# Kernel optimization log

Measured on AMD Instinct MI355X. Metric: run time of the kernel, lower is better.

The kernel has to match this reference:

```python
import jax, jax.numpy as jnp
import numpy as np
from jax import lax

N_CLASSES = 10
GTG_ITER = 30
GTG_TOL = 1e-3
PLB = 0.5
EPS = 1e-8
B = 4096
INTERM = 128
CHANNELS = [64, 128, 256, 512]
SIZES = [8, 8, 4, 4]
EMB_DIM = 512


def setup_inputs() -> dict:
    key = jax.random.key(0)
    ks = jax.random.split(key, 16)
    inp = {}
    for i, (c, s) in enumerate(zip(CHANNELS, SIZES)):
        inp[f"feat{i}"] = jax.random.normal(ks[i], (B, c, s, s), dtype=jnp.float32)
    inp["embedds"] = jax.random.normal(ks[4], (B, EMB_DIM), dtype=jnp.float32)
    inp["outs"] = jax.random.normal(ks[5], (B, N_CLASSES), dtype=jnp.float32)
    inp["labels"] = jax.random.randint(ks[6], (B,), 0, N_CLASSES)
    for i, c in enumerate(CHANNELS):
        inp[f"ls_w{i}"] = jax.random.normal(ks[7 + i], (c, INTERM), dtype=jnp.float32) / np.sqrt(c).astype(np.float32)
        inp[f"ls_b{i}"] = jnp.zeros((INTERM,), dtype=jnp.float32)
    in_feat = GTG_ITER * N_CLASSES  # 300
    inp["mlp_w1"] = jax.random.normal(ks[11], (in_feat, in_feat // 2), dtype=jnp.float32) / np.sqrt(in_feat).astype(np.float32)
    inp["mlp_b1"] = jnp.zeros((in_feat // 2,), dtype=jnp.float32)
    inp["mlp_w2"] = jax.random.normal(ks[12], (in_feat // 2, in_feat // 4), dtype=jnp.float32) / np.sqrt(in_feat // 2).astype(np.float32)
    inp["mlp_b2"] = jnp.zeros((in_feat // 4,), dtype=jnp.float32)
    inp["mlp_w3"] = jax.random.normal(ks[13], (in_feat // 4 * 4, 1), dtype=jnp.float32) / np.sqrt(in_feat).astype(np.float32)
    inp["mlp_b3"] = jnp.zeros((1,), dtype=jnp.float32)
    return inp


def _make_A(emb):
    # get_A_cos_sim: normalize -> NN^T -> zero diag -> clamp[0,1]
    n = emb / jnp.maximum(jnp.linalg.norm(emb, axis=-1, keepdims=True), 1e-12)
    A = n @ n.T
    A = A * (1.0 - jnp.eye(A.shape[0], dtype=A.dtype))
    A = jnp.clip(A, 0.0, 1.0)
    # threshold strategy 'mean': zero entries below mean(A)
    A = jnp.where(A < jnp.mean(A), 0.0, A)
    # AM_strategy 'diversity': A = 1 - A
    return 1.0 - A


def _gtg(A, X0):
    # graph transduction game; while-loop emulated via scan with a running flag
    def step(carry, _):
        X, running = carry
        mult = X * (A @ X)                                 # [B,C]
        div = mult / (jnp.sum(mult, axis=1, keepdims=True) + EPS)
        X_new = X + div
        div_d = lax.stop_gradient(div)
        ent = -jnp.sum(div_d * jnp.log(div_d + EPS), axis=1)  # entropy, detached
        err = jnp.linalg.norm(div_d - lax.stop_gradient(X))
        X_out = jnp.where(running, X_new, X)
        xs_t = jnp.where(running, X_new, jnp.zeros_like(X_new))
        ent_t = jnp.where(running, ent, jnp.zeros_like(ent))
        return (X_out, jnp.logical_and(running, err > GTG_TOL)), (xs_t, ent_t)

    (_, _), (Xs, ents) = lax.scan(step, (X0, jnp.array(True)), None, length=GTG_ITER)
    return jnp.transpose(Xs, (1, 2, 0)), ents.T  # [B,C,T], [B,T]


def _ls(feat, w, b):
    # AvgPool2d over full spatial + Linear + ReLU
    pooled = jnp.mean(feat, axis=(2, 3))  # [B, n_c]
    return jax.nn.relu(pooled @ w + b)


def _mlp(xs_list, w1, b1, w2, b2, w3, b3):
    outs = []
    for xs in xs_list:
        x = xs.reshape(xs.shape[0], -1)  # [B, C*T], torch .view order
        x = jax.nn.relu(x @ w1 + b1)
        x = jax.nn.relu(x @ w2 + b2)
        outs.append(x)
    return (jnp.concatenate(outs, axis=1) @ w3 + b3)[:, 0]


def _init_X(labels, batch):
    n_lab = int(batch * PLB)
    X0 = jnp.full((batch, N_CLASSES), 1.0 / N_CLASSES, dtype=jnp.float32)
    X0 = X0.at[:n_lab].set(0.0)
    X0 = X0.at[jnp.arange(n_lab), labels[:n_lab]].set(1.0)
    return X0, n_lab


def reference(feat0, feat1, feat2, feat3, embedds, outs, labels,
              ls_w0, ls_b0, ls_w1, ls_b1, ls_w2, ls_b2, ls_w3, ls_b3,
              mlp_w1, mlp_b1, mlp_w2, mlp_b2, mlp_w3, mlp_b3):
    batch = embedds.shape[0]
    X0, n_lab = _init_X(labels, batch)
    feats = [feat0, feat1, feat2, feat3]
    lws = [ls_w0, ls_w1, ls_w2, ls_w3]
    lbs = [ls_b0, ls_b1, ls_b2, ls_b3]
    xs_list = []
    for f, w, b in zip(feats, lws, lbs):
        emb = _ls(f, w, b)
        Xs, _ = _gtg(_make_A(emb), X0)
        xs_list.append(Xs)
    y_pred = _mlp(xs_list, mlp_w1, mlp_b1, mlp_w2, mlp_b2, mlp_w3, mlp_b3)  # [B]
    _, ents = _gtg(_make_A(embedds), X0)
    y_true = jnp.mean(ents, axis=1)  # ent_strategy 'mean'
    labelled_mask = jnp.arange(batch) < n_lab
    return y_pred, y_true, labelled_mask
```

## Files before the change

### kernel.cpp

```cpp
#include <hip/hip_runtime.h>
#include <hip/hip_fp16.h>

typedef _Float16 f16x8 __attribute__((ext_vector_type(8)));
typedef float f32x4 __attribute__((ext_vector_type(4)));
typedef unsigned char uchar;

static __device__ __forceinline__ long long mk64(unsigned lo, unsigned hi)
{
    return (long long)(((unsigned long long)hi << 32) | (unsigned long long)lo);
}

static __device__ __forceinline__ int xfrag_off(int c, int j)
{
    return (j >> 6) * 1024 + (((j >> 3) & 3) * 16 + c) * 16 + ((j >> 5) & 1) * 8 + (j & 7);
}

static __device__ __forceinline__ int xsfrag_off(int row, int k)
{
    return (row >> 4) * 5120 + (k >> 5) * 512 + (((k >> 3) & 3) * 16 + (row & 15)) * 8 + (k & 7);
}

#define T03 0x24201800u
#define T47 0x2E2C2A28u
#define T8B 0x33323130u
#define TCF 0x37363534u

static __device__ __forceinline__ void expand4(unsigned w, unsigned& o0, unsigned& o1)
{
    unsigned even = w & 0x0F0F0F0Fu;
    unsigned odd  = (w >> 4) & 0x0F0F0F0Fu;
    unsigned i_lo = __builtin_amdgcn_perm(odd, even, 0x05010400u);
    unsigned i_hi = __builtin_amdgcn_perm(odd, even, 0x07030602u);
    {
        unsigned i3 = i_lo & 0x07070707u;
        unsigned ta = __builtin_amdgcn_perm(T47, T03, i3);
        unsigned tb = __builtin_amdgcn_perm(TCF, T8B, i3);
        unsigned m  = ((i_lo >> 3) & 0x01010101u) * 0xFFu;
        o0 = ta ^ ((ta ^ tb) & m);
    }
    {
        unsigned i3 = i_hi & 0x07070707u;
        unsigned ta = __builtin_amdgcn_perm(T47, T03, i3);
        unsigned tb = __builtin_amdgcn_perm(TCF, T8B, i3);
        unsigned m  = ((i_hi >> 3) & 0x01010101u) * 0xFFu;
        o1 = ta ^ ((ta ^ tb) & m);
    }
}

__global__ __launch_bounds__(256) void fused_ls_kernel(
    const float* __restrict__ f0, const float* __restrict__ f1,
    const float* __restrict__ f2, const float* __restrict__ f3,
    const float* __restrict__ embedds,
    const float* __restrict__ lw0, const float* __restrict__ lb0,
    const float* __restrict__ lw1, const float* __restrict__ lb1,
    const float* __restrict__ lw2, const float* __restrict__ lb2,
    const float* __restrict__ lw3, const float* __restrict__ lb3,
    __half* __restrict__ N16all, int pbase)
{
    __shared__ float pl[512];
    __shared__ float red[4];
    const int t = threadIdx.x;
    const int p = pbase + (blockIdx.x >> 12);
    const int row = blockIdx.x & 4095;

    if (p == 4) {
        float2 v = *(const float2*)(embedds + (size_t)row * 512 + t * 2);
        float ss = v.x * v.x + v.y * v.y;
        for (int off = 32; off > 0; off >>= 1) ss += __shfl_down(ss, off, 64);
        if ((t & 63) == 0) red[t >> 6] = ss;
        __syncthreads();
        float inv = 1.0f / fmaxf(sqrtf(red[0] + red[1] + red[2] + red[3]), 1e-12f);
        __half2 o;
        o.x = __float2half(v.x * inv);
        o.y = __float2half(v.y * inv);
        *(__half2*)(N16all + 2097152 + (size_t)row * 512 + t * 2) = o;
        return;
    }

    const float* feat; const float* w; const float* b; int C;
    switch (p) {
        case 0:  feat = f0; w = lw0; b = lb0; C = 64;  break;
        case 1:  feat = f1; w = lw1; b = lb1; C = 128; break;
        case 2:  feat = f2; w = lw2; b = lb2; C = 256; break;
        default: feat = f3; w = lw3; b = lb3; C = 512; break;
    }
    const float* fr = feat + (size_t)row * C * ((p < 2) ? 64 : 16);

    if (p == 0) {
        const int c = t >> 2, q = t & 3;
        const float4* src = (const float4*)(fr + c * 64 + q * 16);
        float s = 0.f;
#pragma unroll
        for (int i = 0; i < 4; ++i) { float4 v = src[i]; s += v.x + v.y + v.z + v.w; }
        s += __shfl_xor(s, 1, 64);
        s += __shfl_xor(s, 2, 64);
        if (q == 0) pl[c] = s * (1.0f / 64.f);
    } else if (p == 1) {
        const int c = t >> 1, h = t & 1;
        const float4* src = (const float4*)(fr + c * 64 + h * 32);
        float s = 0.f;
#pragma unroll
        for (int i = 0; i < 8; ++i) { float4 v = src[i]; s += v.x + v.y + v.z + v.w; }
        s += __shfl_xor(s, 1, 64);
        if (h == 0) pl[c] = s * (1.0f / 64.f);
    } else if (p == 2) {
        const float4* src = (const float4*)(fr + t * 16);
        float s = 0.f;
#pragma unroll
        for (int i = 0; i < 4; ++i) { float4 v = src[i]; s += v.x + v.y + v.z + v.w; }
        pl[t] = s * (1.0f / 16.f);
    } else {
#pragma unroll
        for (int cc = 0; cc < 2; ++cc) {
            const int c = t + cc * 256;
            const float4* src = (const float4*)(fr + c * 16);
            float s = 0.f;
#pragma unroll
            for (int i = 0; i < 4; ++i) { float4 v = src[i]; s += v.x + v.y + v.z + v.w; }
            pl[c] = s * (1.0f / 16.f);
        }
    }
    __syncthreads();

    float v = 0.f, ss = 0.f;
    if (t < 128) {
        float acc = b[t];
        for (int k = 0; k < C; ++k) acc = fmaf(pl[k], w[(size_t)k * 128 + t], acc);
        v = fmaxf(acc, 0.f);
        ss = v * v;
        for (int off = 32; off > 0; off >>= 1) ss += __shfl_down(ss, off, 64);
        if ((t & 63) == 0) red[t >> 6] = ss;
    }
    __syncthreads();
    if (t < 128) {
        float inv = 1.0f / fmaxf(sqrtf(red[0] + red[1]), 1e-12f);
        N16all[(size_t)p * 524288 + (size_t)row * 128 + t] = __float2half(v * inv);
    }
}

__global__ __launch_bounds__(256) void a_gemm_all(const __half* __restrict__ N16all,
                                                  __half* __restrict__ A16f,
                                                  float* __restrict__ partials,
                                                  int pbase)
{
    __shared__ __half smem[16384];
    __shared__ float reds[4];
    __half* As = smem;
    __half* Bs = smem + 8192;
    char* Cb = (char*)smem;
    const int t = threadIdx.x;
    const int lane = t & 63, wave = t >> 6;
    const int lp = blockIdx.x >> 10;
    const int p = pbase + lp;
    const int blk = blockIdx.x & 1023;
    const int K = (p == 4) ? 512 : 128;
    const __half* N16 = N16all + ((p == 4) ? 2097152u : (unsigned)p * 524288u);
    const int bx = blk & 31, by = blk >> 5;
    const int wr = wave >> 1, wc = wave & 1;
    const int fr = lane & 15;
    const int g = lane >> 4;
    const int r0 = by * 128, c0 = bx * 128;
    const int sr = t >> 3;
    const int sc = t & 7;

    f32x4 acc[4][4];
#pragma unroll
    for (int i = 0; i < 4; ++i)
#pragma unroll
        for (int j = 0; j < 4; ++j) acc[i][j] = (f32x4){0.f, 0.f, 0.f, 0.f};

    for (int kt = 0; kt < (K >> 6); ++kt) {
        const int kb = kt * 64;
        __syncthreads();
#pragma unroll
        for (int pp = 0; pp < 4; ++pp) {
            const int r = pp * 32 + sr;
            uint4 va = *(const uint4*)(N16 + (size_t)(r0 + r) * K + kb + sc * 8);
            uint4 vb = *(const uint4*)(N16 + (size_t)(c0 + r) * K + kb + sc * 8);
            const int d = r * 64 + ((((sc * 16) ^ ((r & 7) << 4))) >> 1);
            *(uint4*)&As[d] = va;
            *(uint4*)&Bs[d] = vb;
        }
        __syncthreads();
#pragma unroll
        for (int ks = 0; ks < 2; ++ks) {
            const int ko = ((ks * 64 + g * 16) ^ ((fr & 7) << 4)) >> 1;
            f16x8 af[4], bf[4];
#pragma unroll
            for (int i = 0; i < 4; ++i) {
                af[i] = *(const f16x8*)&As[(wr * 64 + i * 16 + fr) * 64 + ko];
                bf[i] = *(const f16x8*)&Bs[(wc * 64 + i * 16 + fr) * 64 + ko];
            }
#pragma unroll
            for (int i = 0; i < 4; ++i)
#pragma unroll
                for (int j = 0; j < 4; ++j)
                    acc[i][j] = __builtin_amdgcn_mfma_f32_16x16x32_f16(af[i], bf[j], acc[i][j], 0, 0, 0);
        }
    }
    __syncthreads();

    float lsum = 0.f;
    const int r4 = g * 4;
#pragma unroll
    for (int i = 0; i < 4; ++i) {
#pragma unroll
        for (int q = 0; q < 4; ++q) {
            const int lr = wr * 64 + i * 16 + r4 + q;
            const int row = r0 + lr;
#pragma unroll
            for (int j = 0; j < 4; ++j) {
                const int lc = wc * 64 + j * 16 + fr;
                const int col = c0 + lc;
                float v = fminf(fmaxf(acc[i][j][q], 0.f), 1.f);
                if (row == col) v = 0.f;
                lsum += v;
                *(__half*)(Cb + lr * 256 + ((lc * 2) ^ ((lr & 7) << 4))) = __float2half(v);
            }
        }
    }
    __syncthreads();

#pragma unroll
    for (int pp = 0; pp < 4; ++pp) {
        const int rbl2 = pp * 4 + (t >> 6);
        const int rbl = rbl2 >> 1, ks2l = rbl2 & 1;
        const int l = t & 63;
        const int lr = rbl * 16 + (l & 15);
        const int e0 = ks2l * 64 + (l >> 4) * 8;
        uint4 v0 = *(const uint4*)(Cb + lr * 256 + ((e0 * 2) ^ ((lr & 7) << 4)));
        uint4 v1 = *(const uint4*)(Cb + lr * 256 + (((e0 + 32) * 2) ^ ((lr & 7) << 4)));
        const size_t rb = (size_t)(by * 8 + rbl);
        const size_t ks2 = (size_t)(bx * 2 + ks2l);
        char* dst = (char*)A16f + (size_t)lp * 33554432 + rb * 131072 + ks2 * 2048 + l * 32;
        *(uint4*)dst = v0;
        *(uint4*)(dst + 16) = v1;
    }

    for (int off = 32; off > 0; off >>= 1) lsum += __shfl_down(lsum, off, 64);
    if (lane == 0) reds[wave] = lsum;
    __syncthreads();
    if (t == 0) partials[lp * 1024 + blk] = reds[0] + reds[1] + reds[2] + reds[3];
}

__global__ __launch_bounds__(256) void mean_all_kernel(const float* __restrict__ partials,
                                                       float* __restrict__ scal)
{
    __shared__ float red[4];
    const int t = threadIdx.x, lp = blockIdx.x;
    float s = 0.f;
    for (int i = t; i < 1024; i += 256) s += partials[lp * 1024 + i];
    for (int off = 32; off > 0; off >>= 1) s += __shfl_down(s, off, 64);
    if ((t & 63) == 0) red[t >> 6] = s;
    __syncthreads();
    if (t == 0) scal[lp] = (red[0] + red[1] + red[2] + red[3]) * (1.0f / 16777216.0f);
}

__global__ __launch_bounds__(256) void abar4_all_kernel(const __half* __restrict__ A16f,
                                                        uchar* __restrict__ A4,
                                                        const float* __restrict__ scal)
{
    const int lp = blockIdx.x >> 12;
    const float mean = scal[lp];
    const size_t i = (size_t)(blockIdx.x & 4095) * 256 + threadIdx.x;
    const __half* src = A16f + (size_t)lp * 16777216 + i * 16;
    uint4 u0 = *(const uint4*)(src);
    uint4 u1 = *(const uint4*)(src + 8);
    __half h[16];
    *(uint4*)h = u0;
    *(uint4*)(h + 8) = u1;
    unsigned d0 = 0, d1 = 0;
#pragma unroll
    for (int k = 0; k < 8; ++k) {
        float a = __half2float(h[k]);
        float v = (a < mean) ? 0.f : a;
        unsigned n = (unsigned)fminf(v * 16.f + 0.5f, 15.f);
        d0 |= n << (4 * k);
    }
#pragma unroll
    for (int k = 0; k < 8; ++k) {
        float a = __half2float(h[8 + k]);
        float v = (a < mean) ? 0.f : a;
        unsigned n = (unsigned)fminf(v * 16.f + 0.5f, 15.f);
        d1 |= n << (4 * k);
    }
    uint2 o; o.x = d0; o.y = d1;
    *(uint2*)(A4 + (size_t)lp * 8388608 + i * 8) = o;
}

__global__ __launch_bounds__(256) void init_kernel(const int* __restrict__ labels,
                                                   uchar* __restrict__ X8_0,
                                                   uchar* __restrict__ X8_1,
                                                   float* __restrict__ X32,
                                                   float* __restrict__ Scol)
{
    __shared__ int hist[16];
    const int blk = blockIdx.x;
    const int t = threadIdx.x;
    const int idx = blk * 256 + t;
    const int p = idx >> 16;
    const int rem = idx & 65535;
    const int c = rem >> 12, j = rem & 4095;
    float v;
    if (c >= 10) v = 0.f;
    else if (j < 2048) v = (labels[j] == c) ? 1.0f : 0.0f;
    else v = 0.1f;
    unsigned pk = __builtin_amdgcn_cvt_pk_fp8_f32(v, v, 0, false);
    X8_0[(size_t)p * 65536 + xfrag_off(c, j)] = (uchar)(pk & 0xff);
    if (c >= 10) X8_1[(size_t)p * 65536 + xfrag_off(c, j)] = 0;
    if (c < 10) X32[((size_t)p * 4096 + j) * 10 + c] = v;

    if (blk == 0) {
        if (t < 16) hist[t] = 0;
        __syncthreads();
        for (int i = t; i < 2048; i += 256) atomicAdd(&hist[labels[i]], 1);
        __syncthreads();
        if (t < 80) {
            const int pp = t >> 4, cc = t & 15;
            Scol[pp * 16 + cc] = (cc < 10) ? ((float)hist[cc] + 204.8f) : 0.f;
        }
    } else if (blk <= 30) {
        if (t < 80) Scol[blk * 80 + t] = 0.f;
    }
}

__global__ __launch_bounds__(256) void wfrag_kernel(const float* __restrict__ w1,
                                                    const float* __restrict__ w2,
                                                    __half* __restrict__ W1f,
                                                    __half* __restrict__ W2f)
{
    int idx = blockIdx.x * 256 + threadIdx.x;
    if (idx < 51200) {
        const int frag = idx >> 9, e9 = idx & 511;
        const int s = frag / 10, j = frag % 10;
        const int g = e9 >> 7, fr = (e9 >> 3) & 15, e = e9 & 7;
        const int k = s * 32 + g * 8 + e, n = j * 16 + fr;
        const float v = (k < 300 && n < 150) ? w1[(size_t)k * 150 + n] : 0.f;
        W1f[idx] = __float2half(v);
    } else if (idx < 64000) {
        const int i2 = idx - 51200;
        const int frag = i2 >> 9, e9 = i2 & 511;
        const int s = frag / 5, j = frag % 5;
        const int g = e9 >> 7, fr = (e9 >> 3) & 15, e = e9 & 7;
        const int k = s * 32 + g * 8 + e, n = j * 16 + fr;
        const float v = (k < 150 && n < 75) ? w2[(size_t)k * 75 + n] : 0.f;
        W2f[i2] = __float2half(v);
    }
}

__global__ __launch_bounds__(256, 5) void gtg8_kernel(
    const uchar* __restrict__ A4f,
    const uchar* __restrict__ X8i, uchar* __restrict__ X8o,
    const float* __restrict__ X32i, float* __restrict__ X32o,
    __half* __restrict__ Xs16f, float* __restrict__ ytacc,
    float* __restrict__ Scol, int it, int pbase)
{
    __shared__ float yred[4][256];
    const int t = threadIdx.x;
    const int lane = t & 63, wave = t >> 6;
    const int p = pbase + (blockIdx.x >> 8);
    const int pl = p - pbase;
    const int rb = blockIdx.x & 255;

    const uchar* Ab = A4f + (size_t)pl * 8388608 + (size_t)rb * 32768
                    + wave * 8192 + lane * 8;
    const uchar* Xb = X8i + (size_t)p * 65536 + wave * 16384 + lane * 16;

    f32x4 acc0 = {0.f, 0.f, 0.f, 0.f};
    f32x4 acc1 = {0.f, 0.f, 0.f, 0.f};
#pragma unroll
    for (int u = 0; u < 16; ++u) {
        uint2 a4 = *(const uint2*)(Ab + u * 512);
        uint4 bv = *(const uint4*)(Xb + u * 1024);
        unsigned e00, e01, e10, e11;
        expand4(a4.x, e00, e01);
        expand4(a4.y, e10, e11);
        acc0 = __builtin_amdgcn_mfma_f32_16x16x32_fp8_fp8(
            mk64(e00, e01), mk64(bv.x, bv.y), acc0, 0, 0, 0);
        acc1 = __builtin_amdgcn_mfma_f32_16x16x32_fp8_fp8(
            mk64(e10, e11), mk64(bv.z, bv.w), acc1, 0, 0, 0);
    }
    {
        const int r4 = (lane >> 4) * 4;
        const int fr = lane & 15;
#pragma unroll
        for (int q = 0; q < 4; ++q)
            yred[wave][(r4 + q) * 16 + fr] = acc0[q] + acc1[q];
    }
    __syncthreads();

    const int r = t >> 4, c = t & 15;
    const int row = rb * 16 + r;
    const float T = yred[0][t] + yred[1][t] + yred[2][t] + yred[3][t];
    const float y = Scol[it * 80 + pl * 16 + c] - T;
    const float x = (c < 10) ? X32i[((size_t)p * 4096 + row) * 10 + c] : 0.f;
    const float m = x * y;
    float s = m;
    s += __shfl_xor(s, 1, 16);
    s += __shfl_xor(s, 2, 16);
    s += __shfl_xor(s, 4, 16);
    s += __shfl_xor(s, 8, 16);
    const float dv = m / (s + 1e-8f);
    const float xn = x + dv;
    if (c < 10) {
        X32o[((size_t)p * 4096 + row) * 10 + c] = xn;
        unsigned pk = __builtin_amdgcn_cvt_pk_fp8_f32(xn, xn, 0, false);
        X8o[(size_t)p * 65536 + xfrag_off(c, row)] = (uchar)(pk & 0xff);
        if (p < 4) {
            const int k = c * 30 + it;
            Xs16f[(size_t)p * 1310720 + xsfrag_off(row, k)] = __float2half(xn);
        }
    }
    if (p == 4) {
        float e = (c < 10) ? (-dv * logf(dv + 1e-8f)) : 0.f;
        e += __shfl_xor(e, 1, 16);
        e += __shfl_xor(e, 2, 16);
        e += __shfl_xor(e, 4, 16);
        e += __shfl_xor(e, 8, 16);
        if (c == 0) {
            float prev = (it == 0) ? 0.f : ytacc[row];
            ytacc[row] = prev + e;
        }
    }

    __syncthreads();
    yred[0][t] = (c < 10) ? xn : 0.f;
    __syncthreads();
    if (t < 10) {
        float sc = 0.f;
#pragma unroll
        for (int rr = 0; rr < 16; ++rr) sc += yred[0][t + rr * 16];
        atomicAdd(&Scol[(it + 1) * 80 + pl * 16 + t], sc);
    }
}

__global__ __launch_bounds__(256) void mlp_mfma_kernel(const __half* __restrict__ Xs16f,
                                                       const __half* __restrict__ W1f,
                                                       const __half* __restrict__ W2f,
                                                       const float* __restrict__ b1,
                                                       const float* __restrict__ b2,
                                                       float* __restrict__ H2)
{
    __shared__ char h1s[4][16 * 384];
    __shared__ float b1s[160];
    __shared__ float b2s[80];
    const int t = threadIdx.x;
    const int lane = t & 63, wave = t >> 6;
    const int fr = lane & 15, g = lane >> 4;
    const int lvl = blockIdx.x >> 6;
    const int rb = (blockIdx.x & 63) * 4 + wave;

    if (t < 160) b1s[t] = (t < 150) ? b1[t] : 0.f;
    else if (t < 240) b2s[t - 160] = (t < 235) ? b2[t - 160] : 0.f;
    __syncthreads();

    const __half* Abase = Xs16f + (size_t)lvl * 1310720 + (size_t)rb * 5120;
    f32x4 acc1[10];
#pragma unroll
    for (int j = 0; j < 10; ++j) acc1[j] = (f32x4){0.f, 0.f, 0.f, 0.f};
#pragma unroll
    for (int s = 0; s < 10; ++s) {
        f16x8 a = *(const f16x8*)(Abase + s * 512 + lane * 8);
#pragma unroll
        for (int j = 0; j < 10; ++j) {
            f16x8 b = *(const f16x8*)(W1f + (s * 10 + j) * 512 + lane * 8);
            acc1[j] = __builtin_amdgcn_mfma_f32_16x16x32_f16(a, b, acc1[j], 0, 0, 0);
        }
    }
    char* hw = h1s[wave];
#pragma unroll
    for (int j = 0; j < 10; ++j) {
#pragma unroll
        for (int q = 0; q < 4; ++q) {
            const int row = g * 4 + q;
            const int col = j * 16 + fr;
            float v = fmaxf(acc1[j][q] + b1s[col], 0.f);
            *(__half*)(hw + row * 384 + ((col * 2) ^ ((row & 7) << 4))) = __float2half(v);
        }
    }
    __syncthreads();

    f32x4 acc2[5];
#pragma unroll
    for (int j = 0; j < 5; ++j) acc2[j] = (f32x4){0.f, 0.f, 0.f, 0.f};
#pragma unroll
    for (int s = 0; s < 5; ++s) {
        f16x8 a = *(const f16x8*)(hw + fr * 384 + ((s * 64 + g * 16) ^ ((fr & 7) << 4)));
#pragma unroll
        for (int j = 0; j < 5; ++j) {
            f16x8 b = *(const f16x8*)(W2f + (s * 5 + j) * 512 + lane * 8);
            acc2[j] = __builtin_amdgcn_mfma_f32_16x16x32_f16(a, b, acc2[j], 0, 0, 0);
        }
    }
#pragma unroll
    for (int j = 0; j < 5; ++j) {
        const int col = j * 16 + fr;
        if (col < 75) {
#pragma unroll
            for (int q = 0; q < 4; ++q) {
                const int row = rb * 16 + g * 4 + q;
                float v = fmaxf(acc2[j][q] + b2s[col], 0.f);
                H2[(size_t)row * 300 + lvl * 75 + col] = v;
            }
        }
    }
}

__global__ __launch_bounds__(256) void final_kernel(const float* __restrict__ H2,
                                                    const float* __restrict__ w3,
                                                    const float* __restrict__ b3,
                                                    const float* __restrict__ ytacc,
                                                    float* __restrict__ out)
{
    __shared__ float w[300];
    const int t = threadIdx.x;
    const int b = blockIdx.x * 256 + t;
    for (int i = t; i < 300; i += 256) w[i] = w3[i];
    __syncthreads();
    float acc = b3[0];
    const float4* row = (const float4*)(H2 + (size_t)b * 300);
    for (int k4 = 0; k4 < 75; ++k4) {
        float4 v = row[k4];
        acc += v.x * w[k4 * 4] + v.y * w[k4 * 4 + 1] + v.z * w[k4 * 4 + 2] + v.w * w[k4 * 4 + 3];
    }
    out[b] = acc;
    out[4096 + b] = ytacc[b] * (1.0f / 30.0f);
    out[2 * 4096 + b] = (b < 2048) ? 1.0f : 0.0f;
}

extern "C" void kernel_launch(void* const* d_in, const int* in_sizes, int n_in,
                              void* d_out, int out_size, void* d_ws, size_t ws_size,
                              hipStream_t stream)
{
    (void)in_sizes; (void)n_in; (void)out_size;

    const float* feats[4] = {(const float*)d_in[0], (const float*)d_in[1],
                             (const float*)d_in[2], (const float*)d_in[3]};
    const float* embedds = (const float*)d_in[4];
    const int* labels = (const int*)d_in[6];
    const float* lsw[4] = {(const float*)d_in[7], (const float*)d_in[9],
                           (const float*)d_in[11], (const float*)d_in[13]};
    const float* lsb[4] = {(const float*)d_in[8], (const float*)d_in[10],
                           (const float*)d_in[12], (const float*)d_in[14]};
    const float* w1 = (const float*)d_in[15];
    const float* b1 = (const float*)d_in[16];
    const float* w2 = (const float*)d_in[17];
    const float* b2 = (const float*)d_in[18];
    const float* w3 = (const float*)d_in[19];
    const float* b3 = (const float*)d_in[20];

    const bool fused = ws_size >= 236000000ULL;
    const size_t A4_BYTES  = fused ? 41943040ULL : 8388608ULL;
    const size_t A16_BYTES = fused ? 167772160ULL : 33554432ULL;

    char* ws = (char*)d_ws;
    uchar* A4       = (uchar*)(ws);
    __half* A16f    = (__half*)(ws + A4_BYTES);
    char* base      = ws + A4_BYTES + A16_BYTES;
    __half* N16all  = (__half*)(base);
    uchar* Xt8      = (uchar*)(base + 8388608);
    float* X32      = (float*)(base + 9043968);
    __half* Xs16f   = (__half*)(base + 10682368);
    float* H2       = (float*)(base + 21168128);
    float* ytacc    = (float*)(base + 26083328);
    float* partials = (float*)(base + 26099712);
    float* scal     = (float*)(base + 26120192);
    float* Scol     = (float*)(base + 26120448);
    __half* W1f     = (__half*)(base + 26136832);
    __half* W2f     = (__half*)(base + 26239232);

    uchar* Xt8b[2] = {Xt8, Xt8 + 327680};
    float* X32b[2] = {X32, X32 + 204800};
    float* out = (float*)d_out;

    auto run_iters = [&](const uchar* Ab4, int pbase, int nprob) {
        init_kernel<<<1280, 256, 0, stream>>>(labels, Xt8b[0], Xt8b[1], X32b[0], Scol);
        for (int it = 0; it < 30; ++it) {
            const int i = it & 1, o = i ^ 1;
            gtg8_kernel<<<nprob * 256, 256, 0, stream>>>(
                Ab4, Xt8b[i], Xt8b[o], X32b[i], X32b[o], Xs16f, ytacc, Scol, it, pbase);
        }
    };

    wfrag_kernel<<<250, 256, 0, stream>>>(w1, w2, W1f, W2f);
    hipMemsetAsync(Xs16f, 0, 10485760, stream);

    if (fused) {
        fused_ls_kernel<<<5 * 4096, 256, 0, stream>>>(
            feats[0], feats[1], feats[2], feats[3], embedds,
            lsw[0], lsb[0], lsw[1], lsb[1], lsw[2], lsb[2], lsw[3], lsb[3],
            N16all, 0);
        a_gemm_all<<<5 * 1024, 256, 0, stream>>>(N16all, A16f, partials, 0);
        mean_all_kernel<<<5, 256, 0, stream>>>(partials, scal);
        abar4_all_kernel<<<5 * 4096, 256, 0, stream>>>(A16f, A4, scal);
        run_iters(A4, 0, 5);
    } else {
        for (int p = 0; p < 5; ++p) {
            fused_ls_kernel<<<4096, 256, 0, stream>>>(
                feats[0], feats[1], feats[2], feats[3], embedds,
                lsw[0], lsb[0], lsw[1], lsb[1], lsw[2], lsb[2], lsw[3], lsb[3],
                N16all, p);
            a_gemm_all<<<1024, 256, 0, stream>>>(N16all, A16f, partials, p);
            mean_all_kernel<<<1, 256, 0, stream>>>(partials, scal);
            abar4_all_kernel<<<4096, 256, 0, stream>>>(A16f, A4, scal);
            run_iters(A4, p, 1);
        }
    }

    mlp_mfma_kernel<<<256, 256, 0, stream>>>(Xs16f, W1f, W2f, b1, b2, H2);
    final_kernel<<<16, 256, 0, stream>>>(H2, w3, b3, ytacc, out);
}
```

Measured before the change: 770.5 us.

## Process 16 rows per block in fused_ls_kernel to reuse weight loads

```diff
diff --git a/kernel.cpp b/kernel.cpp
--- a/kernel.cpp
+++ b/kernel.cpp
@@ -57,84 +57,102 @@
     const float* __restrict__ lw3, const float* __restrict__ lb3,
     __half* __restrict__ N16all, int pbase)
 {
-    __shared__ float pl[512];
-    __shared__ float red[4];
+    __shared__ float pl[16][512];
+    __shared__ float red[16][2];
     const int t = threadIdx.x;
-    const int p = pbase + (blockIdx.x >> 12);
-    const int row = blockIdx.x & 4095;
+    const int p = pbase + (blockIdx.x >> 8);
+    const int row0 = (blockIdx.x & 255) * 16;
 
     if (p == 4) {
-        float2 v = *(const float2*)(embedds + (size_t)row * 512 + t * 2);
-        float ss = v.x * v.x + v.y * v.y;
-        for (int off = 32; off > 0; off >>= 1) ss += __shfl_down(ss, off, 64);
-        if ((t & 63) == 0) red[t >> 6] = ss;
-        __syncthreads();
-        float inv = 1.0f / fmaxf(sqrtf(red[0] + red[1] + red[2] + red[3]), 1e-12f);
-        __half2 o;
-        o.x = __float2half(v.x * inv);
-        o.y = __float2half(v.y * inv);
-        *(__half2*)(N16all + 2097152 + (size_t)row * 512 + t * 2) = o;
+        const int r = t >> 4, q = t & 15;
+        const int row = row0 + r;
+        const float4* src = (const float4*)(embedds + (size_t)row * 512 + q * 32);
+        float4 v[8];
+        float ss = 0.f;
+#pragma unroll
+        for (int i = 0; i < 8; ++i) {
+            v[i] = src[i];
+            ss += v[i].x * v[i].x + v[i].y * v[i].y + v[i].z * v[i].z + v[i].w * v[i].w;
+        }
+        ss += __shfl_xor(ss, 1, 16);
+        ss += __shfl_xor(ss, 2, 16);
+        ss += __shfl_xor(ss, 4, 16);
+        ss += __shfl_xor(ss, 8, 16);
+        const float inv = 1.0f / fmaxf(sqrtf(ss), 1e-12f);
+        __half out[32];
+#pragma unroll
+        for (int i = 0; i < 8; ++i) {
+            out[i * 4 + 0] = __float2half(v[i].x * inv);
+            out[i * 4 + 1] = __float2half(v[i].y * inv);
+            out[i * 4 + 2] = __float2half(v[i].z * inv);
+            out[i * 4 + 3] = __float2half(v[i].w * inv);
+        }
+        __half* dst = N16all + 2097152 + (size_t)row * 512 + q * 32;
+#pragma unroll
+        for (int i = 0; i < 4; ++i)
+            *(uint4*)(dst + i * 8) = *(uint4*)(out + i * 8);
         return;
     }
 
-    const float* feat; const float* w; const float* b; int C;
+    const float* feat; const float* w; const float* b; int C, lc, S2;
     switch (p) {
-        case 0:  feat = f0; w = lw0; b = lb0; C = 64;  break;
-        case 1:  feat = f1; w = lw1; b = lb1; C = 128; break;
-        case 2:  feat = f2; w = lw2; b = lb2; C = 256; break;
-        default: feat = f3; w = lw3; b = lb3; C = 512; break;
-    }
-    const float* fr = feat + (size_t)row * C * ((p < 2) ? 64 : 16);
-
-    if (p == 0) {
-        const int c = t >> 2, q = t & 3;
-        const float4* src = (const float4*)(fr + c * 64 + q * 16);
+        case 0:  feat = f0; w = lw0; b = lb0; C = 64;  lc = 6; S2 = 64; break;
+        case 1:  feat = f1; w = lw1; b = lb1; C = 128; lc = 7; S2 = 64; break;
+        case 2:  feat = f2; w = lw2; b = lb2; C = 256; lc = 8; S2 = 16; break;
+        default: feat = f3; w = lw3; b = lb3; C = 512; lc = 9; S2 = 16; break;
+    }
+
+    const float inv_s2 = 1.0f / (float)S2;
+    for (int ci = t; ci < (C << 4); ci += 256) {
+        const int r = ci >> lc, ch = ci & (C - 1);
+        const float4* src = (const float4*)(feat + ((size_t)(row0 + r) * C + ch) * S2);
         float s = 0.f;
-#pragma unroll
-        for (int i = 0; i < 4; ++i) { float4 v = src[i]; s += v.x + v.y + v.z + v.w; }
-        s += __shfl_xor(s, 1, 64);
-        s += __shfl_xor(s, 2, 64);
-        if (q == 0) pl[c] = s * (1.0f / 64.f);
-    } else if (p == 1) {
-        const int c = t >> 1, h = t & 1;
-        const float4* src = (const float4*)(fr + c * 64 + h * 32);
-        float s = 0.f;
-#pragma unroll
-        for (int i = 0; i < 8; ++i) { float4 v = src[i]; s += v.x + v.y + v.z + v.w; }
-        s += __shfl_xor(s, 1, 64);
-        if (h == 0) pl[c] = s * (1.0f / 64.f);
-    } else if (p == 2) {
-        const float4* src = (const float4*)(fr + t * 16);
-        float s = 0.f;
-#pragma unroll
-        for (int i = 0; i < 4; ++i) { float4 v = src[i]; s += v.x + v.y + v.z + v.w; }
-        pl[t] = s * (1.0f / 16.f);
-    } else {
-#pragma unroll
-        for (int cc = 0; cc < 2; ++cc) {
-            const int c = t + cc * 256;
-            const float4* src = (const float4*)(fr + c * 16);
-            float s = 0.f;
+        if (S2 == 64) {
+#pragma unroll
+            for (int i = 0; i < 16; ++i) { float4 v = src[i]; s += v.x + v.y + v.z + v.w; }
+        } else {
 #pragma unroll
             for (int i = 0; i < 4; ++i) { float4 v = src[i]; s += v.x + v.y + v.z + v.w; }
-            pl[c] = s * (1.0f / 16.f);
-        }
-    }
-    __syncthreads();
-
-    float v = 0.f, ss = 0.f;
-    if (t < 128) {
-        float acc = b[t];
-        for (int k = 0; k < C; ++k) acc = fmaf(pl[k], w[(size_t)k * 128 + t], acc);
-        v = fmaxf(acc, 0.f);
-        ss = v * v;
-        for (int off = 32; off > 0; off >>= 1) ss += __shfl_down(ss, off, 64);
-        if ((t & 63) == 0) red[t >> 6] = ss;
-    }
-    __syncthreads();
-    if (t < 128) {
-        float inv = 1.0f / fmaxf(sqrtf(red[0] + red[1]), 1e-12f);
-        N16all[(size_t)p * 524288 + (size_t)row * 128 + t] = __float2half(v * inv);
+        }
+        pl[r][ch] = s * inv_s2;
+    }
+    __syncthreads();
+
+    const int col = t & 127, half = t >> 7;
+    const int wavepart = (t >> 6) & 1;
+    float acc[8];
+#pragma unroll
+    for (int r = 0; r < 8; ++r) acc[r] = b[col];
+#pragma unroll 4
+    for (int k = 0; k < C; ++k) {
+        const float wv = w[(size_t)k * 128 + col];
+#pragma unroll
+        for (int r = 0; r < 8; ++r) acc[r] = fmaf(pl[half * 8 + r][k], wv, acc[r]);
+    }
+    float ssq[8];
+#pragma unroll
+    for (int r = 0; r < 8; ++r) {
+        acc[r] = fmaxf(acc[r], 0.f);
+        float q = acc[r] * acc[r];
+        q += __shfl_xor(q, 1, 64);
+        q += __shfl_xor(q, 2, 64);
+        q += __shfl_xor(q, 4, 64);
+        q += __shfl_xor(q, 8, 64);
+        q += __shfl_xor(q, 16, 64);
+        q += __shfl_xor(q, 32, 64);
+        ssq[r] = q;
+    }
+    if ((t & 63) == 0) {
+#pragma unroll
+        for (int r = 0; r < 8; ++r) red[half * 8 + r][wavepart] = ssq[r];
+    }
+    __syncthreads();
+#pragma unroll
+    for (int r = 0; r < 8; ++r) {
+        const int row = half * 8 + r;
+        const float inv = 1.0f / fmaxf(sqrtf(red[row][0] + red[row][1]), 1e-12f);
+        N16all[(size_t)p * 524288 + (size_t)(row0 + row) * 128 + col] =
+            __float2half(acc[r] * inv);
     }
 }
 
@@ -210,12 +228,12 @@
             const int row = r0 + lr;
 #pragma unroll
             for (int j = 0; j < 4; ++j) {
-                const int lc = wc * 64 + j * 16 + fr;
-                const int col = c0 + lc;
+                const int lc2 = wc * 64 + j * 16 + fr;
+                const int col = c0 + lc2;
                 float v = fminf(fmaxf(acc[i][j][q], 0.f), 1.f);
                 if (row == col) v = 0.f;
                 lsum += v;
-                *(__half*)(Cb + lr * 256 + ((lc * 2) ^ ((lr & 7) << 4))) = __float2half(v);
+                *(__half*)(Cb + lr * 256 + ((lc2 * 2) ^ ((lr & 7) << 4))) = __float2half(v);
             }
         }
     }
@@ -586,7 +604,7 @@
     hipMemsetAsync(Xs16f, 0, 10485760, stream);
 
     if (fused) {
-        fused_ls_kernel<<<5 * 4096, 256, 0, stream>>>(
+        fused_ls_kernel<<<5 * 256, 256, 0, stream>>>(
             feats[0], feats[1], feats[2], feats[3], embedds,
             lsw[0], lsb[0], lsw[1], lsb[1], lsw[2], lsb[2], lsw[3], lsb[3],
             N16all, 0);
@@ -596,7 +614,7 @@
         run_iters(A4, 0, 5);
     } else {
         for (int p = 0; p < 5; ++p) {
-            fused_ls_kernel<<<4096, 256, 0, stream>>>(
+            fused_ls_kernel<<<256, 256, 0, stream>>>(
                 feats[0], feats[1], feats[2], feats[3], embedds,
                 lsw[0], lsb[0], lsw[1], lsb[1], lsw[2], lsb[2], lsw[3], lsb[3],
                 N16all, p);
```

Result: no change. 769.9 us (-0.1%).
